# Kernel tuning notes

Hardware: AMD Instinct MI355X
Metric: run time of the kernel (lower is better)

The kernel has to match this reference:

```python
import jax, jax.numpy as jnp
import numpy as np
import math


def cos_map(N):
    # DCT-II basis: weight[n, x] = cos(n*pi*(x+0.5)/N) * sqrt(2/N), row 0 scaled by 1/sqrt(2)
    wx = (jnp.arange(N, dtype=jnp.float32) + 0.5) / N
    wn = jnp.arange(N, dtype=jnp.float32)[:, None]
    w = jnp.cos(wn * wx[None, :] * jnp.pi) * math.sqrt(2.0 / N)
    return w.at[0, :].multiply(1.0 / math.sqrt(2.0))


def decay_map(H, W):
    wn = jnp.linspace(0.0, jnp.pi, H + 1)[:H][:, None]
    wm = jnp.linspace(0.0, jnp.pi, W + 1)[:W][None, :]
    return jnp.exp(-(wn ** 2 + wm ** 2))  # [H, W]


def layer_norm(x, g, b, eps=1e-5):
    mu = jnp.mean(x, axis=-1, keepdims=True)
    var = jnp.mean(jnp.square(x - mu), axis=-1, keepdims=True)
    return (x - mu) * jax.lax.rsqrt(var + eps) * g + b


def depthwise_conv3x3(x, w, b):
    # x: [B,C,H,W], w: [C,1,3,3] (groups=C), padding=1
    out = jax.lax.conv_general_dilated(
        x, w, window_strides=(1, 1), padding=((1, 1), (1, 1)),
        dimension_numbers=('NCHW', 'OIHW', 'NCHW'), feature_group_count=x.shape[1])
    return out + b[None, :, None, None]


def setup_inputs() -> dict:
    key = jax.random.key(0)
    ks = jax.random.split(key, 10)
    B, C, H, W = 16, 384, 64, 64
    x = jax.random.normal(ks[0], (B, C, H, W), jnp.float32)
    freq_embed = jax.random.normal(ks[1], (B, H, W, C), jnp.float32)
    dw_w = jax.random.normal(ks[2], (C, 1, 3, 3), jnp.float32) * 0.1
    dw_b = jax.random.normal(ks[3], (C,), jnp.float32) * 0.02
    lin_w = jax.random.normal(ks[4], (2 * C, C), jnp.float32) * 0.02
    lin_b = jnp.zeros((2 * C,), jnp.float32)
    tok_w = jax.random.normal(ks[5], (C, C), jnp.float32) * 0.02
    tok_b = jnp.zeros((C,), jnp.float32)
    ln_g = jnp.ones((C,), jnp.float32)
    ln_b = jnp.zeros((C,), jnp.float32)
    out_w = jax.random.normal(ks[6], (C, C), jnp.float32) * 0.02
    out_b = jnp.zeros((C,), jnp.float32)
    c = jnp.ones((1,), jnp.float32)
    alpha = jnp.ones((1,), jnp.float32) * 0.1
    return dict(x=x, freq_embed=freq_embed, dw_w=dw_w, dw_b=dw_b, lin_w=lin_w,
                lin_b=lin_b, tok_w=tok_w, tok_b=tok_b, ln_g=ln_g, ln_b=ln_b,
                out_w=out_w, out_b=out_b, c=c, alpha=alpha)


def reference(x, freq_embed, dw_w, dw_b, lin_w, lin_b, tok_w, tok_b,
              ln_g, ln_b, out_w, out_b, c, alpha):
    B, C, H, W = x.shape
    eps = 1e-8
    xd = depthwise_conv3x3(x, dw_w, dw_b)                       # [B,C,H,W]
    xcl = jnp.transpose(xd, (0, 2, 3, 1))                       # [B,H,W,C]
    xz = xcl @ lin_w.T + lin_b                                  # [B,H,W,2C]
    xs, z = jnp.split(xz, 2, axis=-1)
    Wn = cos_map(H)                                             # [H,H] (freq n, space h)
    Wm = cos_map(W)                                             # [W,W]
    # DCT2D: A(n,m) = sum_{h,w} Wn[n,h] Wm[m,w] phi(h,w)
    Xf = jnp.einsum('nh,bhwc->bnwc', Wn, xs)
    Xf = jnp.einsum('mw,bnwc->bnmc', Wm, Xf)                    # [B,H,W,C] freq domain
    x_u0 = Xf
    x_v0 = Xf  # original computes DCT2D(x) twice (identical)
    # learned time / decay modulation
    t = jax.nn.gelu(freq_embed @ tok_w.T + tok_b, approximate=False)  # [B,H,W,C]
    c_t = c * t
    cos_term = jnp.cos(c_t)
    sin_term = jnp.sin(c_t) / (c + eps)
    final = cos_term * x_u0 + sin_term * (x_v0 + (alpha / 2.0) * x_u0)
    wexp = decay_map(H, W)                                      # [H,W]
    final = final * jnp.power(wexp[None, :, :, None], t)        # freq-dependent decay e^{-(n^2+m^2)t}
    # IDCT2D: u(h,w) = sum_{n,m} Wn[n,h] Wm[m,w] A(n,m)
    xo = jnp.einsum('nh,bnmc->bhmc', Wn, final)
    xo = jnp.einsum('mw,bhmc->bhwc', Wm, xo)                    # [B,H,W,C]
    xo = layer_norm(xo, ln_g, ln_b)
    xo = xo * jax.nn.silu(z)
    out = xo @ out_w.T + out_b                                  # [B,H,W,C]
    return out
```

## Files before the change

kernel.cpp:

```cpp
#include <hip/hip_runtime.h>
#include <hip/hip_bf16.h>
#include <math.h>


typedef __attribute__((ext_vector_type(8))) short short8;
typedef __attribute__((ext_vector_type(4))) float floatx4;

#define PIF 3.14159265358979323846f

__device__ __forceinline__ short f2bf(float f) {
    union { float f; unsigned u; } v; v.f = f;
    unsigned r = v.u + 0x7fffu + ((v.u >> 16) & 1u);
    return (short)(r >> 16);
}
__device__ __forceinline__ float bf2f(short s) {
    union { unsigned u; float f; } v;
    v.u = ((unsigned)(unsigned short)s) << 16;
    return v.f;
}
__device__ __forceinline__ float fast_erf(float x) {
    float ax = fabsf(x);
    float t = 1.0f / fmaf(0.3275911f, ax, 1.0f);
    float poly = t * fmaf(t, fmaf(t, fmaf(t, fmaf(t, 1.061405429f, -1.453152027f),
                                          1.421413741f), -0.284496736f), 0.254829592f);
    float er = 1.0f - poly * __expf(-ax * ax);
    return copysignf(er, x);
}

__device__ __forceinline__ void gload16(const short* g, short* l) {
    __builtin_amdgcn_global_load_lds(
        (const __attribute__((address_space(1))) void*)g,
        (__attribute__((address_space(3))) void*)l, 16, 0, 0);
}

__global__ __launch_bounds__(256) void k_f2bf(const float* __restrict__ src,
                                              short* __restrict__ dst, int n) {
    int i = (blockIdx.x * 256 + threadIdx.x) * 4;
    if (i < n) {
        float4 f = *(const float4*)(src + i);
        short4 o;
        o.x = f2bf(f.x); o.y = f2bf(f.y); o.z = f2bf(f.z); o.w = f2bf(f.w);
        *(short4*)(dst + i) = o;
    }
}

__global__ __launch_bounds__(256) void k_build_dct(short* __restrict__ wn,
                                                   short* __restrict__ wnt) {
    int i = blockIdx.x * 256 + threadIdx.x;
    if (i < 4096) {
        int n = i >> 6, h = i & 63;
        float v = cosf((float)n * ((float)h + 0.5f) * (PIF / 64.0f)) * sqrtf(2.0f / 64.0f);
        if (n == 0) v *= 0.70710678118654752f;
        short b = f2bf(v);
        wn[n * 64 + h]  = b;
        wnt[h * 64 + n] = b;
    }
}

__global__ __launch_bounds__(256) void k_conv(const float* __restrict__ x,
                                              const float* __restrict__ w,
                                              const float* __restrict__ bias,
                                              short* __restrict__ out) {
    __shared__ float sp[4096];
    int bc = blockIdx.x;
    int c = bc % 384;
    int tid = threadIdx.x;
    const float* xp = x + (size_t)bc * 4096;
    for (int i = 0; i < 4; i++) {
        int e = i * 1024 + tid * 4;
        *(float4*)(sp + e) = *(const float4*)(xp + e);
    }
    float wt[9];
    #pragma unroll
    for (int j = 0; j < 9; j++) wt[j] = w[c * 9 + j];
    float bv = bias[c];
    __syncthreads();
    short* op = out + (size_t)bc * 4096;
    for (int i = 0; i < 16; i++) {
        int hw = i * 256 + tid;
        int h = hw >> 6, ww = hw & 63;
        float acc = bv;
        #pragma unroll
        for (int dh = 0; dh < 3; dh++) {
            int ih = h + dh - 1;
            if (ih < 0 || ih > 63) continue;
            #pragma unroll
            for (int dw = 0; dw < 3; dw++) {
                int iw = ww + dw - 1;
                if (iw < 0 || iw > 63) continue;
                acc += sp[ih * 64 + iw] * wt[dh * 3 + dw];
            }
        }
        op[hw] = f2bf(acc);
    }
}

__global__ __launch_bounds__(256) void k_pl2tok(const short* __restrict__ src,
                                                short* __restrict__ dst) {
    __shared__ short tile[64 * 66];
    int ct = blockIdx.x, ht = blockIdx.y, b = blockIdx.z;
    int tid = threadIdx.x;
    const short* sp = src + ((size_t)b * 384 + ct * 64) * 4096 + ht * 64;
    for (int i = 0; i < 16; i++) {
        int idx = i * 256 + tid;
        int r = idx >> 6, col = idx & 63;
        tile[r * 66 + col] = sp[(size_t)r * 4096 + col];
    }
    __syncthreads();
    short* dp = dst + ((size_t)b * 4096 + ht * 64) * 384 + ct * 64;
    for (int i = 0; i < 16; i++) {
        int idx = i * 256 + tid;
        int r = idx >> 6, col = idx & 63;
        dp[(size_t)r * 384 + col] = tile[col * 66 + r];
    }
}

__device__ __forceinline__ void mm_core(const short* __restrict__ A,
                                        const short* __restrict__ Bw,
                                        int row_base, int col_base,
                                        short* smem, floatx4 (&acc)[4][4]) {
    const int K = 384;
    int tid = threadIdx.x;
    int wid = tid >> 6, lane = tid & 63;
    int quad = lane >> 4, l16 = lane & 15;
    int rowh = (wid >> 1) * 64, colh = (wid & 1) * 64;
    short* ldsA = smem;
    short* ldsB = smem + 8192;
    const short* ga = A + (size_t)row_base * K;
    const short* gb = Bw + (size_t)col_base * K;

    int q0 = tid, q1 = 256 + tid;
    int r0 = q0 >> 2, o0 = ((q0 & 3) ^ ((q0 >> 3) & 3)) * 8;
    int r1 = q1 >> 2, o1 = ((q1 & 3) ^ ((q1 >> 3) & 3)) * 8;
    short* la0 = ldsA + (wid * 64) * 8;
    short* la1 = ldsA + (256 + wid * 64) * 8;
    short* lb0 = ldsB + (wid * 64) * 8;
    short* lb1 = ldsB + (256 + wid * 64) * 8;

    auto stage = [&](int ks, int buf) {
        int k0 = ks * 32;
        gload16(ga + (size_t)r0 * K + k0 + o0, la0 + buf * 4096);
        gload16(ga + (size_t)r1 * K + k0 + o1, la1 + buf * 4096);
        gload16(gb + (size_t)r0 * K + k0 + o0, lb0 + buf * 4096);
        gload16(gb + (size_t)r1 * K + k0 + o1, lb1 + buf * 4096);
    };

    int ksw = (quad ^ ((l16 >> 1) & 3)) * 8;

    stage(0, 0);
    __syncthreads();
    #pragma unroll 2
    for (int ks = 0; ks < 12; ++ks) {
        int cur = ks & 1;
        if (ks < 11) stage(ks + 1, cur ^ 1);
        short8 af[4], bfr[4];
        #pragma unroll
        for (int s = 0; s < 4; s++) {
            af[s]  = *(const short8*)(ldsA + cur * 4096 + (rowh + s * 16 + l16) * 32 + ksw);
            bfr[s] = *(const short8*)(ldsB + cur * 4096 + (colh + s * 16 + l16) * 32 + ksw);
        }
        #pragma unroll
        for (int i = 0; i < 4; i++)
            #pragma unroll
            for (int j = 0; j < 4; j++)
                acc[i][j] = __builtin_amdgcn_mfma_f32_16x16x32_bf16(af[i], bfr[j], acc[i][j], 0, 0, 0);
        __syncthreads();
    }
}

__global__ __launch_bounds__(256) void k_gemm_split(const short* __restrict__ A,
                                                    const short* __restrict__ Bw,
                                                    const float* __restrict__ bias,
                                                    short* __restrict__ xs_pl,
                                                    short* __restrict__ z_tok) {
    __shared__ __align__(16) short smem[17408];
    int bid = blockIdx.x;
    int xcd = bid & 7, local = bid >> 3;
    int bx = local % 6;
    int by = xcd * 64 + local / 6;
    int row_base = by * 128, col_base = bx * 128;
    int tid = threadIdx.x;
    int wid = tid >> 6, lane = tid & 63, quad = lane >> 4, l16 = lane & 15;
    int rowh = (wid >> 1) * 64, colh = (wid & 1) * 64;

    floatx4 zero = {0.f, 0.f, 0.f, 0.f};
    floatx4 acc[4][4];
    #pragma unroll
    for (int i = 0; i < 4; i++)
        #pragma unroll
        for (int j = 0; j < 4; j++) acc[i][j] = zero;

    mm_core(A, Bw, row_base, col_base, smem, acc);

    if (bx < 3) {
        #pragma unroll
        for (int i = 0; i < 4; i++)
            #pragma unroll
            for (int j = 0; j < 4; j++) {
                int cl = colh + j * 16 + l16;
                float bs = bias[col_base + cl];
                #pragma unroll
                for (int r = 0; r < 4; r++) {
                    int rl = rowh + i * 16 + quad * 4 + r;
                    smem[cl * 136 + rl] = f2bf(acc[i][j][r] + bs);
                }
            }
        __syncthreads();
        int t0 = row_base;
        int b = t0 >> 12, hw0 = t0 & 4095;
        for (int it = 0; it < 8; it++) {
            int q = it * 256 + tid;
            int cl = q >> 4, t8 = (q & 15) * 8;
            short8 vv = *(const short8*)(smem + cl * 136 + t8);
            int c = col_base + cl;
            *(short8*)(xs_pl + ((size_t)b * 384 + c) * 4096 + hw0 + t8) = vv;
        }
    } else {
        #pragma unroll
        for (int i = 0; i < 4; i++)
            #pragma unroll
            for (int j = 0; j < 4; j++) {
                int col = col_base + colh + j * 16 + l16;
                float bs = bias[col];
                int cc = col - 384;
                #pragma unroll
                for (int r = 0; r < 4; r++) {
                    int row = row_base + rowh + i * 16 + quad * 4 + r;
                    z_tok[(size_t)row * 384 + cc] = f2bf(acc[i][j][r] + bs);
                }
            }
    }
}

__global__ __launch_bounds__(256) void k_gemm_mod(const short* __restrict__ A,
                                                  const short* __restrict__ Bw,
                                                  const float* __restrict__ bias,
                                                  short* __restrict__ Dpl,
                                                  const float* __restrict__ cp,
                                                  const float* __restrict__ ap) {
    __shared__ __align__(16) short smem[17408];
    int bid = blockIdx.x;
    int xcd = bid & 7, local = bid >> 3;
    int bx = local % 3;
    int by = xcd * 64 + local / 3;
    int row_base = by * 128, col_base = bx * 128;
    int tid = threadIdx.x;
    int wid = tid >> 6, lane = tid & 63, quad = lane >> 4, l16 = lane & 15;
    int rowh = (wid >> 1) * 64, colh = (wid & 1) * 64;

    floatx4 zero = {0.f, 0.f, 0.f, 0.f};
    floatx4 acc[4][4];
    #pragma unroll
    for (int i = 0; i < 4; i++)
        #pragma unroll
        for (int j = 0; j < 4; j++) acc[i][j] = zero;

    mm_core(A, Bw, row_base, col_base, smem, acc);

    float cv = cp[0], av = ap[0];
    float inv_c = 1.0f / (cv + 1e-8f);
    float gfac = 1.0f + 0.5f * av;
    #pragma unroll
    for (int i = 0; i < 4; i++) {
        #pragma unroll
        for (int j = 0; j < 4; j++) {
            int cl = colh + j * 16 + l16;
            float bs = bias[col_base + cl];
            #pragma unroll
            for (int r = 0; r < 4; r++) {
                int rl = rowh + i * 16 + quad * 4 + r;
                int row = row_base + rl;
                float v = acc[i][j][r] + bs;
                float t = 0.5f * v * (1.0f + fast_erf(v * 0.70710678118654752f));
                float ct = cv * t;
                float sn, cs;
                __sincosf(ct, &sn, &cs);
                float fac = cs + sn * inv_c * gfac;
                int nn = (row >> 6) & 63, mm = row & 63;
                float wnf = (float)nn * (PIF / 64.0f);
                float wmf = (float)mm * (PIF / 64.0f);
                float mod = fac * __expf(-(wnf * wnf + wmf * wmf) * t);
                smem[cl * 136 + rl] = f2bf(mod);
            }
        }
    }
    __syncthreads();
    int t0 = row_base;
    int b = t0 >> 12, hw0 = t0 & 4095;
    for (int it = 0; it < 8; it++) {
        int q = it * 256 + tid;
        int cl = q >> 4, t8 = (q & 15) * 8;
        short8 vv = *(const short8*)(smem + cl * 136 + t8);
        int c = col_base + cl;
        *(short8*)(Dpl + ((size_t)b * 384 + c) * 4096 + hw0 + t8) = vv;
    }
}

__global__ __launch_bounds__(256) void k_spectral(const short* __restrict__ xs,
                                                  const short* __restrict__ mod,
                                                  const short* __restrict__ wn,
                                                  const short* __restrict__ wnt,
                                                  short* __restrict__ xo) {
    __shared__ short sWn[4096], sWt[4096], sP[4096], sM[4096], sT[4096];
    int bc = blockIdx.x;
    int tid = threadIdx.x;
    int wid = tid >> 6, lane = tid & 63, quad = lane >> 4, l16 = lane & 15;
    const short* xp = xs + (size_t)bc * 4096;
    const short* mp = mod + (size_t)bc * 4096;
    floatx4 zero = {0.f, 0.f, 0.f, 0.f};

    for (int i = 0; i < 2; i++) {
        int e = i * 2048 + tid * 8;
        *(short8*)(sWn + e) = *(const short8*)(wn + e);
        *(short8*)(sWt + e) = *(const short8*)(wnt + e);
        *(short8*)(sM + e)  = *(const short8*)(mp + e);
        short8 pv = *(const short8*)(xp + e);
        int h = e >> 6, w0 = e & 63;
        #pragma unroll
        for (int j = 0; j < 8; j++) sP[(w0 + j) * 64 + h] = pv[j];
    }
    __syncthreads();

    int mrow = wid * 16;
    floatx4 acc[4];

    #pragma unroll
    for (int j = 0; j < 4; j++) acc[j] = zero;
    #pragma unroll
    for (int ks = 0; ks < 2; ks++) {
        int k0 = ks * 32 + quad * 8;
        short8 a = *(const short8*)(sWn + (mrow + l16) * 64 + k0);
        #pragma unroll
        for (int j = 0; j < 4; j++) {
            short8 b = *(const short8*)(sP + (j * 16 + l16) * 64 + k0);
            acc[j] = __builtin_amdgcn_mfma_f32_16x16x32_bf16(a, b, acc[j], 0, 0, 0);
        }
    }
    #pragma unroll
    for (int j = 0; j < 4; j++)
        #pragma unroll
        for (int r = 0; r < 4; r++)
            sT[(mrow + quad * 4 + r) * 64 + j * 16 + l16] = f2bf(acc[j][r]);
    __syncthreads();

    #pragma unroll
    for (int j = 0; j < 4; j++) acc[j] = zero;
    #pragma unroll
    for (int ks = 0; ks < 2; ks++) {
        int k0 = ks * 32 + quad * 8;
        short8 a = *(const short8*)(sT + (mrow + l16) * 64 + k0);
        #pragma unroll
        for (int j = 0; j < 4; j++) {
            short8 b = *(const short8*)(sWn + (j * 16 + l16) * 64 + k0);
            acc[j] = __builtin_amdgcn_mfma_f32_16x16x32_bf16(a, b, acc[j], 0, 0, 0);
        }
    }
    __syncthreads();
    #pragma unroll
    for (int j = 0; j < 4; j++)
        #pragma unroll
        for (int r = 0; r < 4; r++) {
            int n = mrow + quad * 4 + r, m = j * 16 + l16;
            float v = acc[j][r] * bf2f(sM[n * 64 + m]);
            sP[m * 64 + n] = f2bf(v);
        }
    __syncthreads();

    #pragma unroll
    for (int j = 0; j < 4; j++) acc[j] = zero;
    #pragma unroll
    for (int ks = 0; ks < 2; ks++) {
        int k0 = ks * 32 + quad * 8;
        short8 a = *(const short8*)(sWt + (mrow + l16) * 64 + k0);
        #pragma unroll
        for (int j = 0; j < 4; j++) {
            short8 b = *(const short8*)(sP + (j * 16 + l16) * 64 + k0);
            acc[j] = __builtin_amdgcn_mfma_f32_16x16x32_bf16(a, b, acc[j], 0, 0, 0);
        }
    }
    __syncthreads();
    #pragma unroll
    for (int j = 0; j < 4; j++)
        #pragma unroll
        for (int r = 0; r < 4; r++)
            sT[(mrow + quad * 4 + r) * 64 + j * 16 + l16] = f2bf(acc[j][r]);
    __syncthreads();

    #pragma unroll
    for (int j = 0; j < 4; j++) acc[j] = zero;
    #pragma unroll
    for (int ks = 0; ks < 2; ks++) {
        int k0 = ks * 32 + quad * 8;
        short8 a = *(const short8*)(sT + (mrow + l16) * 64 + k0);
        #pragma unroll
        for (int j = 0; j < 4; j++) {
            short8 b = *(const short8*)(sWt + (j * 16 + l16) * 64 + k0);
            acc[j] = __builtin_amdgcn_mfma_f32_16x16x32_bf16(a, b, acc[j], 0, 0, 0);
        }
    }
    short* op = xo + (size_t)bc * 4096;
    #pragma unroll
    for (int j = 0; j < 4; j++)
        #pragma unroll
        for (int r = 0; r < 4; r++) {
            int h = mrow + quad * 4 + r, w = j * 16 + l16;
            op[h * 64 + w] = f2bf(acc[j][r]);
        }
}

__global__ __launch_bounds__(256) void k_ln_silu(const short* __restrict__ xo,
                                                 const short* __restrict__ z,
                                                 const float* __restrict__ g,
                                                 const float* __restrict__ bb,
                                                 short* __restrict__ y) {
    int wid = threadIdx.x >> 6, lane = threadIdx.x & 63;
    size_t token = (size_t)blockIdx.x * 4 + wid;
    const short* xp = xo + token * 384;
    float v[6];
    float s = 0.f, sq = 0.f;
    #pragma unroll
    for (int j = 0; j < 6; j++) {
        v[j] = bf2f(xp[lane + j * 64]);
        s += v[j]; sq += v[j] * v[j];
    }
    #pragma unroll
    for (int m = 1; m < 64; m <<= 1) {
        s  += __shfl_xor(s, m, 64);
        sq += __shfl_xor(sq, m, 64);
    }
    float mu = s * (1.0f / 384.0f);
    float var = sq * (1.0f / 384.0f) - mu * mu;
    float rstd = rsqrtf(var + 1e-5f);
    const short* zp = z + token * 384;
    short* yp = y + token * 384;
    #pragma unroll
    for (int j = 0; j < 6; j++) {
        int cc = lane + j * 64;
        float zz = bf2f(zp[cc]);
        float sil = zz / (1.f + __expf(-zz));
        float o = (v[j] - mu) * rstd * g[cc] + bb[cc];
        yp[cc] = f2bf(o * sil);
    }
}

__global__ __launch_bounds__(256) void k_gemm_f32out(const short* __restrict__ A,
                                                     const short* __restrict__ Bw,
                                                     const float* __restrict__ bias,
                                                     float* __restrict__ D) {
    __shared__ __align__(16) short smem[17408];
    const int N = 384;
    int bid = blockIdx.x;
    int xcd = bid & 7, local = bid >> 3;
    int bx = local % 3;
    int by = xcd * 64 + local / 3;
    int row_base = by * 128, col_base = bx * 128;
    int tid = threadIdx.x;
    int wid = tid >> 6, lane = tid & 63, quad = lane >> 4, l16 = lane & 15;
    int rowh = (wid >> 1) * 64, colh = (wid & 1) * 64;

    floatx4 zero = {0.f, 0.f, 0.f, 0.f};
    floatx4 acc[4][4];
    #pragma unroll
    for (int i = 0; i < 4; i++)
        #pragma unroll
        for (int j = 0; j < 4; j++) acc[i][j] = zero;

    mm_core(A, Bw, row_base, col_base, smem, acc);

    #pragma unroll
    for (int i = 0; i < 4; i++) {
        #pragma unroll
        for (int j = 0; j < 4; j++) {
            int col = col_base + colh + j * 16 + l16;
            float bs = bias[col];
            #pragma unroll
            for (int r = 0; r < 4; r++) {
                int row = row_base + rowh + i * 16 + quad * 4 + r;
                D[(size_t)row * N + col] = acc[i][j][r] + bs;
            }
        }
    }
}

extern "C" void kernel_launch(void* const* d_in, const int* in_sizes, int n_in,
                              void* d_out, int out_size, void* d_ws, size_t ws_size,
                              hipStream_t stream) {
    const float* x     = (const float*)d_in[0];
    const float* freq  = (const float*)d_in[1];
    const float* dw_w  = (const float*)d_in[2];
    const float* dw_b  = (const float*)d_in[3];
    const float* lin_w = (const float*)d_in[4];
    const float* lin_b = (const float*)d_in[5];
    const float* tok_w = (const float*)d_in[6];
    const float* tok_b = (const float*)d_in[7];
    const float* ln_g  = (const float*)d_in[8];
    const float* ln_b  = (const float*)d_in[9];
    const float* out_w = (const float*)d_in[10];
    const float* out_b = (const float*)d_in[11];
    const float* cp    = (const float*)d_in[12];
    const float* ap    = (const float*)d_in[13];
    float* out = (float*)d_out;
    (void)in_sizes; (void)n_in; (void)ws_size;

    const size_t TC = (size_t)65536 * 384;
    short* bufA = (short*)d_out;
    short* bufB = (short*)d_out + TC;

    char* ws = (char*)d_ws;
    size_t off = 0;
    auto alloc = [&](size_t bytes) {
        char* p = ws + off; off += (bytes + 255) & ~(size_t)255; return p;
    };
    short* wn_bf   = (short*)alloc(4096 * 2);
    short* wnt_bf  = (short*)alloc(4096 * 2);
    short* linw_bf = (short*)alloc((size_t)294912 * 2);
    short* tokw_bf = (short*)alloc((size_t)147456 * 2);
    short* outw_bf = (short*)alloc((size_t)147456 * 2);
    short* bufC    = (short*)alloc(TC * 2);
    short* bufE    = (short*)alloc(TC * 2);

    k_f2bf<<<288, 256, 0, stream>>>(lin_w, linw_bf, 294912);
    k_f2bf<<<144, 256, 0, stream>>>(tok_w, tokw_bf, 147456);
    k_f2bf<<<144, 256, 0, stream>>>(out_w, outw_bf, 147456);
    k_build_dct<<<16, 256, 0, stream>>>(wn_bf, wnt_bf);

    k_conv<<<6144, 256, 0, stream>>>(x, dw_w, dw_b, bufE);
    k_pl2tok<<<dim3(6, 64, 16), 256, 0, stream>>>(bufE, bufC);
    k_gemm_split<<<3072, 256, 0, stream>>>(bufC, linw_bf, lin_b,
                                           bufA, bufB);
    k_f2bf<<<24576, 256, 0, stream>>>(freq, bufE, 25165824);
    k_gemm_mod<<<1536, 256, 0, stream>>>(bufE, tokw_bf, tok_b,
                                         bufC, cp, ap);
    k_spectral<<<6144, 256, 0, stream>>>(bufA, bufC, wn_bf, wnt_bf,
                                         bufE);
    k_pl2tok<<<dim3(6, 64, 16), 256, 0, stream>>>(bufE, bufA);
    k_ln_silu<<<16384, 256, 0, stream>>>(bufA, bufB, ln_g, ln_b, bufC);
    k_gemm_f32out<<<1536, 256, 0, stream>>>(bufC, outw_bf, out_b, out);
}
```

Before: 544.9 us.

## Fuse fp32-to-bf16 conversion into token GEMM and transpose into LayerNorm-SiLU

The token-projection GEMM now reads the fp32 freq_embed directly, converting to bf16 in registers before writing to LDS. This removes a separate conversion kernel and its round trip through a 50 MB intermediate. The planar-to-token transpose after the spectral stage is folded into a new LayerNorm+SiLU kernel, which transposes a 64-token tile through shared memory before normalising. The fp32 A loads double the GEMM's global read traffic for that operand. The LDS transpose writes are scattered by column and may cause bank conflicts.

```diff
diff --git a/kernel.cpp b/kernel.cpp
--- a/kernel.cpp
+++ b/kernel.cpp
@@ -164,6 +164,79 @@
             #pragma unroll
             for (int j = 0; j < 4; j++)
                 acc[i][j] = __builtin_amdgcn_mfma_f32_16x16x32_bf16(af[i], bfr[j], acc[i][j], 0, 0, 0);
+        __syncthreads();
+    }
+}
+
+__device__ __forceinline__ void mm_core_f32a(const float* __restrict__ Af,
+                                             const short* __restrict__ Bw,
+                                             int row_base, int col_base,
+                                             short* smem, floatx4 (&acc)[4][4]) {
+    const int K = 384;
+    int tid = threadIdx.x;
+    int wid = tid >> 6, lane = tid & 63;
+    int quad = lane >> 4, l16 = lane & 15;
+    int rowh = (wid >> 1) * 64, colh = (wid & 1) * 64;
+    short* ldsA = smem;
+    short* ldsB = smem + 8192;
+    const float* ga = Af + (size_t)row_base * K;
+    const short* gb = Bw + (size_t)col_base * K;
+
+    int q0 = tid, q1 = 256 + tid;
+    int r0 = q0 >> 2, o0 = ((q0 & 3) ^ ((q0 >> 3) & 3)) * 8;
+    int r1 = q1 >> 2, o1 = ((q1 & 3) ^ ((q1 >> 3) & 3)) * 8;
+    short* lb0 = ldsB + (wid * 64) * 8;
+    short* lb1 = ldsB + (256 + wid * 64) * 8;
+
+    auto stageB = [&](int ks, int buf) {
+        int k0 = ks * 32;
+        gload16(gb + (size_t)r0 * K + k0 + o0, lb0 + buf * 4096);
+        gload16(gb + (size_t)r1 * K + k0 + o1, lb1 + buf * 4096);
+    };
+    auto loadA = [&](int ks, float4 (&fa)[4]) {
+        int k0 = ks * 32;
+        const float* p0 = ga + (size_t)r0 * K + k0 + o0;
+        const float* p1 = ga + (size_t)r1 * K + k0 + o1;
+        fa[0] = *(const float4*)(p0);
+        fa[1] = *(const float4*)(p0 + 4);
+        fa[2] = *(const float4*)(p1);
+        fa[3] = *(const float4*)(p1 + 4);
+    };
+    auto cvt2 = [&](const float4& a, const float4& b) {
+        short8 s;
+        s[0] = f2bf(a.x); s[1] = f2bf(a.y); s[2] = f2bf(a.z); s[3] = f2bf(a.w);
+        s[4] = f2bf(b.x); s[5] = f2bf(b.y); s[6] = f2bf(b.z); s[7] = f2bf(b.w);
+        return s;
+    };
+    auto writeA = [&](int buf, const float4 (&fa)[4]) {
+        *(short8*)(ldsA + buf * 4096 + q0 * 8) = cvt2(fa[0], fa[1]);
+        *(short8*)(ldsA + buf * 4096 + q1 * 8) = cvt2(fa[2], fa[3]);
+    };
+
+    int ksw = (quad ^ ((l16 >> 1) & 3)) * 8;
+
+    float4 fa[4];
+    loadA(0, fa);
+    stageB(0, 0);
+    writeA(0, fa);
+    __syncthreads();
+    #pragma unroll 2
+    for (int ks = 0; ks < 12; ++ks) {
+        int cur = ks & 1;
+        float4 fn[4];
+        if (ks < 11) { loadA(ks + 1, fn); stageB(ks + 1, cur ^ 1); }
+        short8 af[4], bfr[4];
+        #pragma unroll
+        for (int s = 0; s < 4; s++) {
+            af[s]  = *(const short8*)(ldsA + cur * 4096 + (rowh + s * 16 + l16) * 32 + ksw);
+            bfr[s] = *(const short8*)(ldsB + cur * 4096 + (colh + s * 16 + l16) * 32 + ksw);
+        }
+        #pragma unroll
+        for (int i = 0; i < 4; i++)
+            #pragma unroll
+            for (int j = 0; j < 4; j++)
+                acc[i][j] = __builtin_amdgcn_mfma_f32_16x16x32_bf16(af[i], bfr[j], acc[i][j], 0, 0, 0);
+        if (ks < 11) writeA(cur ^ 1, fn);
         __syncthreads();
     }
 }
@@ -232,7 +305,7 @@
     }
 }
 
-__global__ __launch_bounds__(256) void k_gemm_mod(const short* __restrict__ A,
+__global__ __launch_bounds__(256) void k_gemm_mod(const float* __restrict__ A,
                                                   const short* __restrict__ Bw,
                                                   const float* __restrict__ bias,
                                                   short* __restrict__ Dpl,
@@ -255,7 +328,7 @@
         #pragma unroll
         for (int j = 0; j < 4; j++) acc[i][j] = zero;
 
-    mm_core(A, Bw, row_base, col_base, smem, acc);
+    mm_core_f32a(A, Bw, row_base, col_base, smem, acc);
 
     float cv = cp[0], av = ap[0];
     float inv_c = 1.0f / (cv + 1e-8f);
@@ -408,38 +481,65 @@
         }
 }
 
-__global__ __launch_bounds__(256) void k_ln_silu(const short* __restrict__ xo,
-                                                 const short* __restrict__ z,
-                                                 const float* __restrict__ g,
-                                                 const float* __restrict__ bb,
-                                                 short* __restrict__ y) {
-    int wid = threadIdx.x >> 6, lane = threadIdx.x & 63;
-    size_t token = (size_t)blockIdx.x * 4 + wid;
-    const short* xp = xo + token * 384;
-    float v[6];
+__global__ __launch_bounds__(256) void k_lnfuse(const short* __restrict__ xo_pl,
+                                                const short* __restrict__ z,
+                                                const float* __restrict__ g,
+                                                const float* __restrict__ bb,
+                                                short* __restrict__ y) {
+    __shared__ short tile[64 * 392];
+    int tid = threadIdx.x;
+    int t0 = blockIdx.x * 64;
+    int b = t0 >> 12, hw0 = t0 & 4095;
+
+    for (int it = 0; it < 12; it++) {
+        int m = it * 256 + tid;
+        int c = m >> 3, t8 = (m & 7) * 8;
+        short8 v = *(const short8*)(xo_pl + ((size_t)b * 384 + c) * 4096 + hw0 + t8);
+        #pragma unroll
+        for (int j = 0; j < 8; j++) tile[(t8 + j) * 392 + c] = v[j];
+    }
+    __syncthreads();
+
+    int t = tid >> 2, qd = tid & 3;
+    int cbase = qd * 96;
+    const short* trow = tile + t * 392 + cbase;
     float s = 0.f, sq = 0.f;
     #pragma unroll
-    for (int j = 0; j < 6; j++) {
-        v[j] = bf2f(xp[lane + j * 64]);
-        s += v[j]; sq += v[j] * v[j];
-    }
-    #pragma unroll
-    for (int m = 1; m < 64; m <<= 1) {
-        s  += __shfl_xor(s, m, 64);
-        sq += __shfl_xor(sq, m, 64);
-    }
+    for (int i = 0; i < 12; i++) {
+        short8 xv = *(const short8*)(trow + i * 8);
+        #pragma unroll
+        for (int j = 0; j < 8; j++) {
+            float f = bf2f(xv[j]);
+            s += f; sq += f * f;
+        }
+    }
+    s  += __shfl_xor(s, 1, 64);  s  += __shfl_xor(s, 2, 64);
+    sq += __shfl_xor(sq, 1, 64); sq += __shfl_xor(sq, 2, 64);
     float mu = s * (1.0f / 384.0f);
     float var = sq * (1.0f / 384.0f) - mu * mu;
     float rstd = rsqrtf(var + 1e-5f);
-    const short* zp = z + token * 384;
-    short* yp = y + token * 384;
-    #pragma unroll
-    for (int j = 0; j < 6; j++) {
-        int cc = lane + j * 64;
-        float zz = bf2f(zp[cc]);
-        float sil = zz / (1.f + __expf(-zz));
-        float o = (v[j] - mu) * rstd * g[cc] + bb[cc];
-        yp[cc] = f2bf(o * sil);
+
+    const short* zp = z + (size_t)(t0 + t) * 384 + cbase;
+    short* yp = y + (size_t)(t0 + t) * 384 + cbase;
+    #pragma unroll
+    for (int i = 0; i < 12; i++) {
+        short8 xv = *(const short8*)(trow + i * 8);
+        short8 zv = *(const short8*)(zp + i * 8);
+        float4 g0 = *(const float4*)(g + cbase + i * 8);
+        float4 g1 = *(const float4*)(g + cbase + i * 8 + 4);
+        float4 b0 = *(const float4*)(bb + cbase + i * 8);
+        float4 b1 = *(const float4*)(bb + cbase + i * 8 + 4);
+        float gv[8] = {g0.x, g0.y, g0.z, g0.w, g1.x, g1.y, g1.z, g1.w};
+        float bv[8] = {b0.x, b0.y, b0.z, b0.w, b1.x, b1.y, b1.z, b1.w};
+        short8 ov;
+        #pragma unroll
+        for (int j = 0; j < 8; j++) {
+            float zz = bf2f(zv[j]);
+            float sil = zz / (1.f + __expf(-zz));
+            float o = (bf2f(xv[j]) - mu) * rstd * gv[j] + bv[j];
+            ov[j] = f2bf(o * sil);
+        }
+        *(short8*)(yp + i * 8) = ov;
     }
 }
 
@@ -528,12 +628,10 @@
     k_pl2tok<<<dim3(6, 64, 16), 256, 0, stream>>>(bufE, bufC);
     k_gemm_split<<<3072, 256, 0, stream>>>(bufC, linw_bf, lin_b,
                                            bufA, bufB);
-    k_f2bf<<<24576, 256, 0, stream>>>(freq, bufE, 25165824);
-    k_gemm_mod<<<1536, 256, 0, stream>>>(bufE, tokw_bf, tok_b,
+    k_gemm_mod<<<1536, 256, 0, stream>>>(freq, tokw_bf, tok_b,
                                          bufC, cp, ap);
     k_spectral<<<6144, 256, 0, stream>>>(bufA, bufC, wn_bf, wnt_bf,
                                          bufE);
-    k_pl2tok<<<dim3(6, 64, 16), 256, 0, stream>>>(bufE, bufA);
-    k_ln_silu<<<16384, 256, 0, stream>>>(bufA, bufB, ln_g, ln_b, bufC);
+    k_lnfuse<<<1024, 256, 0, stream>>>(bufE, bufB, ln_g, ln_b, bufC);
     k_gemm_f32out<<<1536, 256, 0, stream>>>(bufC, outw_bf, out_b, out);
 }
```

New measurement: 576.6 us. 1.06x slower.
